# Optimization experiments

Measured on AMD Instinct MI355X. Metric: run time of the kernel, lower is better.

Reference implementation:

```python
import jax, jax.numpy as jnp
import numpy as np


def setup_inputs() -> dict:
    key = jax.random.key(0)
    ks = jax.random.split(key, 8)
    B, T, I, H, O = 4096, 2048, 4, 20, 4
    s_ih = 1.0 / np.sqrt(H)
    return {
        "x": jax.random.normal(ks[0], (B, T, I), dtype=jnp.float32),
        "h0": jax.random.normal(ks[1], (B, H), dtype=jnp.float32),
        "W_ih": jax.random.uniform(ks[2], (H, I), jnp.float32, -s_ih, s_ih),
        "W_hh": jax.random.uniform(ks[3], (H, H), jnp.float32, -s_ih, s_ih),
        "b_ih": jax.random.uniform(ks[4], (H,), jnp.float32, -s_ih, s_ih),
        "b_hh": jax.random.uniform(ks[5], (H,), jnp.float32, -s_ih, s_ih),
        "fc_w": jax.random.uniform(ks[6], (O, H), jnp.float32, -s_ih, s_ih),
        "fc_b": jax.random.uniform(ks[7], (O,), jnp.float32, -s_ih, s_ih),
    }


def reference(x, h0, W_ih, W_hh, b_ih, b_hh, fc_w, fc_b):
    # x: [B, T, I] batch_first; vanilla tanh RNN recurrence.
    # Precompute the input projection for all timesteps in one GEMM.
    xi = jnp.einsum("bti,hi->tbh", x, W_ih) + b_ih + b_hh  # [T, B, H]

    def step(h, xt):
        h = jnp.tanh(xt + h @ W_hh.T)  # [B, H]
        return h, None

    h_last, _ = jax.lax.scan(step, h0, xi)
    # Module takes last timestep only, then Linear(H -> 4).
    return h_last @ fc_w.T + fc_b  # [B, 4]
```

## Files before the change

### kernel.cpp

```cpp
#include <hip/hip_runtime.h>
#include <cstddef>


typedef float f32x2 __attribute__((ext_vector_type(2)));
typedef float f32x4 __attribute__((ext_vector_type(4)));

constexpr int Tn   = 2048;
constexpr int Hn   = 20;
constexpr int EPB  = 16;
constexpr int SB   = 16;
constexpr int NBLK = Tn / SB;

__global__ __launch_bounds__(256, 1) void rnn_fwd(
    const float* __restrict__ x,
    const float* __restrict__ h0,
    const float* __restrict__ W_ih,
    const float* __restrict__ W_hh,
    const float* __restrict__ b_ih,
    const float* __restrict__ b_hh,
    const float* __restrict__ fc_w,
    const float* __restrict__ fc_b,
    float* __restrict__ out)
{
    __shared__ __align__(16) f32x4 xlds[2][EPB][SB + 1];
    __shared__ float hsh[EPB][24];

    const int tid = threadIdx.x;
    const int j   = tid & 15;
    const int e   = tid >> 4;
    const int b   = blockIdx.x * EPB + e;
    const int uB  = 16 + (j & 3);

    const float S = 2.88539008177792681472f;

    f32x2 w2[16];
#pragma unroll
    for (int r = 0; r < 16; ++r) {
        const int k = (j - r) & 15;
        w2[r] = f32x2{S * W_hh[j * Hn + k], S * W_hh[uB * Hn + k]};
    }
    f32x2 wq2[4], xiw[4];
#pragma unroll
    for (int c = 0; c < 4; ++c) {
        wq2[c] = f32x2{S * W_hh[j * Hn + 16 + c], S * W_hh[uB * Hn + 16 + c]};
        xiw[c] = f32x2{S * W_ih[j * 4 + c],       S * W_ih[uB * 4 + c]};
    }
    f32x2 bias2 = f32x2{S * (b_ih[j] + b_hh[j]), S * (b_ih[uB] + b_hh[uB])};

    float hA = h0[b * Hn + j];
    float hB = h0[b * Hn + uB];

    const f32x4* __restrict__ xp =
        reinterpret_cast<const f32x4*>(x) + (size_t)b * Tn;

#define DPPM " row_mask:0xf bank_mask:0xf\n\t"
#define PKB  " op_sel:[0,0,0] op_sel_hi:[1,0,1]\n\t"

#define STEP(XV) do {                                                         \
    f32x2 xa_ = __builtin_shufflevector((XV), (XV), 0, 1);                    \
    f32x2 xb_ = __builtin_shufflevector((XV), (XV), 2, 3);                    \
    asm volatile(                                                             \
                 \
  "v_pk_fma_f32 v[46:47], %[x0], %[xa], %[b2]" PKB                            \
  "v_pk_mul_f32 v[48:49], %[x1], %[xa] op_sel:[0,1] op_sel_hi:[1,1]\n\t"      \
  "v_pk_fma_f32 v[46:47], %[x2], %[xb], v[46:47]" PKB                         \
  "v_pk_fma_f32 v[48:49], %[x3], %[xb], v[48:49] op_sel:[0,1,0] op_sel_hi:[1,1,1]\n\t" \
                                \
  "v_mov_b32 v42, %[hA]\n\t"                                                  \
                   \
  "v_mov_b32_dpp v44, %[hA] row_ror:1"  DPPM                                  \
  "v_pk_fma_f32 v[46:47], %[w0], v[42:43], v[46:47]" PKB                      \
  "v_mov_b32_dpp v42, %[hA] row_ror:2"  DPPM                                  \
  "v_pk_fma_f32 v[48:49], %[w1], v[44:45], v[48:49]" PKB                      \
  "v_mov_b32_dpp v44, %[hA] row_ror:3"  DPPM                                  \
  "v_pk_fma_f32 v[46:47], %[w2], v[42:43], v[46:47]" PKB                      \
  "v_mov_b32_dpp v42, %[hA] row_ror:4"  DPPM                                  \
  "v_pk_fma_f32 v[48:49], %[w3], v[44:45], v[48:49]" PKB                      \
  "v_mov_b32_dpp v44, %[hA] row_ror:5"  DPPM                                  \
  "v_pk_fma_f32 v[46:47], %[w4], v[42:43], v[46:47]" PKB                      \
  "v_mov_b32_dpp v42, %[hA] row_ror:6"  DPPM                                  \
  "v_pk_fma_f32 v[48:49], %[w5], v[44:45], v[48:49]" PKB                      \
  "v_mov_b32_dpp v44, %[hA] row_ror:7"  DPPM                                  \
  "v_pk_fma_f32 v[46:47], %[w6], v[42:43], v[46:47]" PKB                      \
  "v_mov_b32_dpp v42, %[hA] row_ror:8"  DPPM                                  \
  "v_pk_fma_f32 v[48:49], %[w7], v[44:45], v[48:49]" PKB                      \
  "v_mov_b32_dpp v44, %[hA] row_ror:9"  DPPM                                  \
  "v_pk_fma_f32 v[46:47], %[w8], v[42:43], v[46:47]" PKB                      \
  "v_mov_b32_dpp v42, %[hA] row_ror:10" DPPM                                  \
  "v_pk_fma_f32 v[48:49], %[w9], v[44:45], v[48:49]" PKB                      \
  "v_mov_b32_dpp v44, %[hA] row_ror:11" DPPM                                  \
  "v_pk_fma_f32 v[46:47], %[w10], v[42:43], v[46:47]" PKB                     \
  "v_mov_b32_dpp v42, %[hA] row_ror:12" DPPM                                  \
  "v_pk_fma_f32 v[48:49], %[w11], v[44:45], v[48:49]" PKB                     \
  "v_mov_b32_dpp v44, %[hA] row_ror:13" DPPM                                  \
  "v_pk_fma_f32 v[46:47], %[w12], v[42:43], v[46:47]" PKB                     \
  "v_mov_b32_dpp v42, %[hA] row_ror:14" DPPM                                  \
  "v_pk_fma_f32 v[48:49], %[w13], v[44:45], v[48:49]" PKB                     \
  "v_mov_b32_dpp v44, %[hA] row_ror:15" DPPM                                  \
  "v_pk_fma_f32 v[46:47], %[w14], v[42:43], v[46:47]" PKB                     \
  "v_mov_b32_dpp v42, %[hB] quad_perm:[0,0,0,0]" DPPM                         \
  "v_pk_fma_f32 v[48:49], %[w15], v[44:45], v[48:49]" PKB                     \
  "v_mov_b32_dpp v44, %[hB] quad_perm:[1,1,1,1]" DPPM                         \
  "v_pk_fma_f32 v[46:47], %[q0], v[42:43], v[46:47]" PKB                      \
  "v_mov_b32_dpp v42, %[hB] quad_perm:[2,2,2,2]" DPPM                         \
  "v_pk_fma_f32 v[48:49], %[q1], v[44:45], v[48:49]" PKB                      \
  "v_mov_b32_dpp v44, %[hB] quad_perm:[3,3,3,3]" DPPM                         \
  "v_pk_fma_f32 v[46:47], %[q2], v[42:43], v[46:47]" PKB                      \
  "v_pk_fma_f32 v[48:49], %[q3], v[44:45], v[48:49]" PKB                      \
                    \
  "v_pk_add_f32 v[46:47], v[46:47], v[48:49]\n\t"                             \
  "v_exp_f32 v50, v46\n\t"                                                    \
  "v_exp_f32 v51, v47\n\t"                                                    \
  "v_add_f32 v50, 1.0, v50\n\t"                                               \
  "v_add_f32 v51, 1.0, v51\n\t"                                               \
  "v_rcp_f32 v50, v50\n\t"                                                    \
  "v_rcp_f32 v51, v51\n\t"                                                    \
  "v_fma_f32 %[hA], v50, -2.0, 1.0\n\t"                                       \
  "v_fma_f32 %[hB], v51, -2.0, 1.0"                                           \
  : [hA] "+v"(hA), [hB] "+v"(hB)                                              \
  : [xa] "v"(xa_), [xb] "v"(xb_),                                             \
    [w0] "v"(w2[0]),   [w1] "v"(w2[1]),   [w2] "v"(w2[2]),   [w3] "v"(w2[3]), \
    [w4] "v"(w2[4]),   [w5] "v"(w2[5]),   [w6] "v"(w2[6]),   [w7] "v"(w2[7]), \
    [w8] "v"(w2[8]),   [w9] "v"(w2[9]),   [w10] "v"(w2[10]), [w11] "v"(w2[11]),\
    [w12] "v"(w2[12]), [w13] "v"(w2[13]), [w14] "v"(w2[14]), [w15] "v"(w2[15]),\
    [q0] "v"(wq2[0]),  [q1] "v"(wq2[1]),  [q2] "v"(wq2[2]),  [q3] "v"(wq2[3]),\
    [x0] "v"(xiw[0]),  [x1] "v"(xiw[1]),  [x2] "v"(xiw[2]),  [x3] "v"(xiw[3]),\
    [b2] "v"(bias2)                                                           \
  : "v42","v43","v44","v45","v46","v47","v48","v49","v50","v51");             \
} while (0)

    xlds[0][e][j] = xp[j];
    f32x4 q0 = xlds[0][e][0];
    f32x4 q1 = xlds[0][e][1];
    f32x4 q2 = xlds[0][e][2];

    int cur = 0;
#pragma unroll 1
    for (int k = 0; k < NBLK; ++k) {
        const int kn = (k + 1 < NBLK) ? (k + 1) : (NBLK - 1);
        f32x4 xr = xp[kn * SB + j];
        const int nxt = cur ^ 1;
#pragma unroll
        for (int s = 0; s < SB - 3; ++s) {
            f32x4 xv = q0; q0 = q1; q1 = q2;
            q2 = xlds[cur][e][s + 3];
            STEP(xv);
        }
        xlds[nxt][e][j] = xr;
        { f32x4 xv = q0; q0 = q1; q1 = q2; q2 = xlds[nxt][e][0]; STEP(xv); }
        { f32x4 xv = q0; q0 = q1; q1 = q2; q2 = xlds[nxt][e][1]; STEP(xv); }
        { f32x4 xv = q0; q0 = q1; q1 = q2; q2 = xlds[nxt][e][2]; STEP(xv); }
        cur = nxt;
    }
#undef STEP
#undef PKB
#undef DPPM

    hsh[e][j] = hA;
    if (j < 4) hsh[e][16 + j] = hB;
    if (j < 4) {
        float o = fc_b[j];
#pragma unroll
        for (int kk = 0; kk < Hn; ++kk)
            o = __builtin_fmaf(hsh[e][kk], fc_w[j * Hn + kk], o);
        out[b * 4 + j] = o;
    }
}

extern "C" void kernel_launch(void* const* d_in, const int* in_sizes, int n_in,
                              void* d_out, int out_size, void* d_ws, size_t ws_size,
                              hipStream_t stream) {
    const float* x    = (const float*)d_in[0];
    const float* h0   = (const float*)d_in[1];
    const float* W_ih = (const float*)d_in[2];
    const float* W_hh = (const float*)d_in[3];
    const float* b_ih = (const float*)d_in[4];
    const float* b_hh = (const float*)d_in[5];
    const float* fc_w = (const float*)d_in[6];
    const float* fc_b = (const float*)d_in[7];
    float* out = (float*)d_out;

    rnn_fwd<<<dim3(256), dim3(256), 0, stream>>>(x, h0, W_ih, W_hh, b_ih, b_hh,
                                                 fc_w, fc_b, out);
}
```

Baseline: 403.9 us.

## Precompute next step's input projection off the critical path, use four accumulators

Splits each RNN step into a recurrent multiply-accumulate phase and a tail that reduces the partial sums, applies tanh, and immediately seeds the next step's accumulators with that step's input projection and bias. This takes the x·W_ih term off the h-dependent dependency chain. It also spreads the 20 recurrent FMAs across four accumulator pairs instead of two, shortening the serial FMA chain at the cost of extra adds in the reduction. The x prefetch pipeline is shifted by one timestep to match. A risk is that the final x projection computed past the last timestep is wasted work, and the extra accumulator registers add pressure.

```diff
diff --git a/kernel.cpp b/kernel.cpp
--- a/kernel.cpp
+++ b/kernel.cpp
@@ -56,83 +56,98 @@
 #define DPPM " row_mask:0xf bank_mask:0xf\n\t"
 #define PKB  " op_sel:[0,0,0] op_sel_hi:[1,0,1]\n\t"
 
-#define STEP(XV) do {                                                         \
-    f32x2 xa_ = __builtin_shufflevector((XV), (XV), 0, 1);                    \
-    f32x2 xb_ = __builtin_shufflevector((XV), (XV), 2, 3);                    \
+#define STEP_MAC() do {                                                       \
     asm volatile(                                                             \
-                 \
-  "v_pk_fma_f32 v[46:47], %[x0], %[xa], %[b2]" PKB                            \
-  "v_pk_mul_f32 v[48:49], %[x1], %[xa] op_sel:[0,1] op_sel_hi:[1,1]\n\t"      \
-  "v_pk_fma_f32 v[46:47], %[x2], %[xb], v[46:47]" PKB                         \
-  "v_pk_fma_f32 v[48:49], %[x3], %[xb], v[48:49] op_sel:[0,1,0] op_sel_hi:[1,1,1]\n\t" \
-                                \
   "v_mov_b32 v42, %[hA]\n\t"                                                  \
-                   \
   "v_mov_b32_dpp v44, %[hA] row_ror:1"  DPPM                                  \
-  "v_pk_fma_f32 v[46:47], %[w0], v[42:43], v[46:47]" PKB                      \
-  "v_mov_b32_dpp v42, %[hA] row_ror:2"  DPPM                                  \
-  "v_pk_fma_f32 v[48:49], %[w1], v[44:45], v[48:49]" PKB                      \
-  "v_mov_b32_dpp v44, %[hA] row_ror:3"  DPPM                                  \
-  "v_pk_fma_f32 v[46:47], %[w2], v[42:43], v[46:47]" PKB                      \
-  "v_mov_b32_dpp v42, %[hA] row_ror:4"  DPPM                                  \
-  "v_pk_fma_f32 v[48:49], %[w3], v[44:45], v[48:49]" PKB                      \
-  "v_mov_b32_dpp v44, %[hA] row_ror:5"  DPPM                                  \
-  "v_pk_fma_f32 v[46:47], %[w4], v[42:43], v[46:47]" PKB                      \
+  "v_mov_b32_dpp v46, %[hA] row_ror:2"  DPPM                                  \
+  "v_pk_fma_f32 %[P], %[w0], v[42:43], %[P]" PKB                              \
+  "v_mov_b32_dpp v42, %[hA] row_ror:3"  DPPM                                  \
+  "v_pk_fma_f32 %[Q], %[w1], v[44:45], %[Q]" PKB                              \
+  "v_mov_b32_dpp v44, %[hA] row_ror:4"  DPPM                                  \
+  "v_pk_fma_f32 %[R], %[w2], v[46:47], %[R]" PKB                              \
+  "v_mov_b32_dpp v46, %[hA] row_ror:5"  DPPM                                  \
+  "v_pk_fma_f32 %[Sc], %[w3], v[42:43], %[Sc]" PKB                            \
   "v_mov_b32_dpp v42, %[hA] row_ror:6"  DPPM                                  \
-  "v_pk_fma_f32 v[48:49], %[w5], v[44:45], v[48:49]" PKB                      \
+  "v_pk_fma_f32 %[P], %[w4], v[44:45], %[P]" PKB                              \
   "v_mov_b32_dpp v44, %[hA] row_ror:7"  DPPM                                  \
-  "v_pk_fma_f32 v[46:47], %[w6], v[42:43], v[46:47]" PKB                      \
-  "v_mov_b32_dpp v42, %[hA] row_ror:8"  DPPM                                  \
-  "v_pk_fma_f32 v[48:49], %[w7], v[44:45], v[48:49]" PKB                      \
-  "v_mov_b32_dpp v44, %[hA] row_ror:9"  DPPM                                  \
-  "v_pk_fma_f32 v[46:47], %[w8], v[42:43], v[46:47]" PKB                      \
-  "v_mov_b32_dpp v42, %[hA] row_ror:10" DPPM                                  \
-  "v_pk_fma_f32 v[48:49], %[w9], v[44:45], v[48:49]" PKB                      \
-  "v_mov_b32_dpp v44, %[hA] row_ror:11" DPPM                                  \
-  "v_pk_fma_f32 v[46:47], %[w10], v[42:43], v[46:47]" PKB                     \
+  "v_pk_fma_f32 %[Q], %[w5], v[46:47], %[Q]" PKB                              \
+  "v_mov_b32_dpp v46, %[hA] row_ror:8"  DPPM                                  \
+  "v_pk_fma_f32 %[R], %[w6], v[42:43], %[R]" PKB                              \
+  "v_mov_b32_dpp v42, %[hA] row_ror:9"  DPPM                                  \
+  "v_pk_fma_f32 %[Sc], %[w7], v[44:45], %[Sc]" PKB                            \
+  "v_mov_b32_dpp v44, %[hA] row_ror:10" DPPM                                  \
+  "v_pk_fma_f32 %[P], %[w8], v[46:47], %[P]" PKB                              \
+  "v_mov_b32_dpp v46, %[hA] row_ror:11" DPPM                                  \
+  "v_pk_fma_f32 %[Q], %[w9], v[42:43], %[Q]" PKB                              \
   "v_mov_b32_dpp v42, %[hA] row_ror:12" DPPM                                  \
-  "v_pk_fma_f32 v[48:49], %[w11], v[44:45], v[48:49]" PKB                     \
+  "v_pk_fma_f32 %[R], %[w10], v[44:45], %[R]" PKB                             \
   "v_mov_b32_dpp v44, %[hA] row_ror:13" DPPM                                  \
-  "v_pk_fma_f32 v[46:47], %[w12], v[42:43], v[46:47]" PKB                     \
-  "v_mov_b32_dpp v42, %[hA] row_ror:14" DPPM                                  \
-  "v_pk_fma_f32 v[48:49], %[w13], v[44:45], v[48:49]" PKB                     \
-  "v_mov_b32_dpp v44, %[hA] row_ror:15" DPPM                                  \
-  "v_pk_fma_f32 v[46:47], %[w14], v[42:43], v[46:47]" PKB                     \
-  "v_mov_b32_dpp v42, %[hB] quad_perm:[0,0,0,0]" DPPM                         \
-  "v_pk_fma_f32 v[48:49], %[w15], v[44:45], v[48:49]" PKB                     \
-  "v_mov_b32_dpp v44, %[hB] quad_perm:[1,1,1,1]" DPPM                         \
-  "v_pk_fma_f32 v[46:47], %[q0], v[42:43], v[46:47]" PKB                      \
+  "v_pk_fma_f32 %[Sc], %[w11], v[46:47], %[Sc]" PKB                           \
+  "v_mov_b32_dpp v46, %[hA] row_ror:14" DPPM                                  \
+  "v_pk_fma_f32 %[P], %[w12], v[42:43], %[P]" PKB                             \
+  "v_mov_b32_dpp v42, %[hA] row_ror:15" DPPM                                  \
+  "v_pk_fma_f32 %[Q], %[w13], v[44:45], %[Q]" PKB                             \
+  "v_mov_b32_dpp v44, %[hB] quad_perm:[0,0,0,0]" DPPM                         \
+  "v_pk_fma_f32 %[R], %[w14], v[46:47], %[R]" PKB                             \
+  "v_mov_b32_dpp v46, %[hB] quad_perm:[1,1,1,1]" DPPM                         \
+  "v_pk_fma_f32 %[Sc], %[w15], v[42:43], %[Sc]" PKB                           \
   "v_mov_b32_dpp v42, %[hB] quad_perm:[2,2,2,2]" DPPM                         \
-  "v_pk_fma_f32 v[48:49], %[q1], v[44:45], v[48:49]" PKB                      \
+  "v_pk_fma_f32 %[P], %[q0], v[44:45], %[P]" PKB                              \
   "v_mov_b32_dpp v44, %[hB] quad_perm:[3,3,3,3]" DPPM                         \
-  "v_pk_fma_f32 v[46:47], %[q2], v[42:43], v[46:47]" PKB                      \
-  "v_pk_fma_f32 v[48:49], %[q3], v[44:45], v[48:49]" PKB                      \
-                    \
-  "v_pk_add_f32 v[46:47], v[46:47], v[48:49]\n\t"                             \
-  "v_exp_f32 v50, v46\n\t"                                                    \
-  "v_exp_f32 v51, v47\n\t"                                                    \
-  "v_add_f32 v50, 1.0, v50\n\t"                                               \
-  "v_add_f32 v51, 1.0, v51\n\t"                                               \
-  "v_rcp_f32 v50, v50\n\t"                                                    \
-  "v_rcp_f32 v51, v51\n\t"                                                    \
-  "v_fma_f32 %[hA], v50, -2.0, 1.0\n\t"                                       \
-  "v_fma_f32 %[hB], v51, -2.0, 1.0"                                           \
-  : [hA] "+v"(hA), [hB] "+v"(hB)                                              \
-  : [xa] "v"(xa_), [xb] "v"(xb_),                                             \
+  "v_pk_fma_f32 %[Q], %[q1], v[46:47], %[Q]" PKB                              \
+  "v_pk_fma_f32 %[R], %[q2], v[42:43], %[R]" PKB                              \
+  "v_pk_fma_f32 %[Sc], %[q3], v[44:45], %[Sc]"                                \
+  " op_sel:[0,0,0] op_sel_hi:[1,0,1]"                                         \
+  : [P] "+v"(xiP), [Q] "+v"(xiQ), [R] "+v"(xiR), [Sc] "+v"(xiS)               \
+  : [hA] "v"(hA), [hB] "v"(hB),                                               \
     [w0] "v"(w2[0]),   [w1] "v"(w2[1]),   [w2] "v"(w2[2]),   [w3] "v"(w2[3]), \
     [w4] "v"(w2[4]),   [w5] "v"(w2[5]),   [w6] "v"(w2[6]),   [w7] "v"(w2[7]), \
     [w8] "v"(w2[8]),   [w9] "v"(w2[9]),   [w10] "v"(w2[10]), [w11] "v"(w2[11]),\
     [w12] "v"(w2[12]), [w13] "v"(w2[13]), [w14] "v"(w2[14]), [w15] "v"(w2[15]),\
-    [q0] "v"(wq2[0]),  [q1] "v"(wq2[1]),  [q2] "v"(wq2[2]),  [q3] "v"(wq2[3]),\
-    [x0] "v"(xiw[0]),  [x1] "v"(xiw[1]),  [x2] "v"(xiw[2]),  [x3] "v"(xiw[3]),\
+    [q0] "v"(wq2[0]),  [q1] "v"(wq2[1]),  [q2] "v"(wq2[2]),  [q3] "v"(wq2[3]) \
+  : "v42","v43","v44","v45","v46","v47");                                     \
+} while (0)
+
+#define STEP_TAIL(XV) do {                                                    \
+    f32x2 xa_ = __builtin_shufflevector((XV), (XV), 0, 1);                    \
+    f32x2 xb_ = __builtin_shufflevector((XV), (XV), 2, 3);                    \
+    asm volatile(                                                             \
+  "v_pk_add_f32 v[48:49], %[P], %[Q]\n\t"                                     \
+  "v_pk_add_f32 v[50:51], %[R], %[Sc]\n\t"                                    \
+  "v_pk_fma_f32 %[P], %[x0], %[xa], %[b2]" PKB                                \
+  "v_pk_add_f32 v[48:49], v[48:49], v[50:51]\n\t"                             \
+  "v_pk_mul_f32 %[Q], %[x1], %[xa] op_sel:[0,1] op_sel_hi:[1,1]\n\t"          \
+  "v_pk_mul_f32 %[R], %[x2], %[xb] op_sel:[0,0] op_sel_hi:[1,0]\n\t"          \
+  "v_exp_f32 v52, v48\n\t"                                                    \
+  "v_exp_f32 v53, v49\n\t"                                                    \
+  "v_pk_mul_f32 %[Sc], %[x3], %[xb] op_sel:[0,1] op_sel_hi:[1,1]\n\t"         \
+  "v_add_f32 v52, 1.0, v52\n\t"                                               \
+  "v_add_f32 v53, 1.0, v53\n\t"                                               \
+  "v_rcp_f32 v52, v52\n\t"                                                    \
+  "v_rcp_f32 v53, v53\n\t"                                                    \
+  "v_fma_f32 %[hA], v52, -2.0, 1.0\n\t"                                       \
+  "v_fma_f32 %[hB], v53, -2.0, 1.0"                                           \
+  : [hA] "=v"(hA), [hB] "=v"(hB),                                             \
+    [P] "+v"(xiP), [Q] "+v"(xiQ), [R] "+v"(xiR), [Sc] "+v"(xiS)               \
+  : [xa] "v"(xa_), [xb] "v"(xb_),                                             \
+    [x0] "v"(xiw[0]), [x1] "v"(xiw[1]), [x2] "v"(xiw[2]), [x3] "v"(xiw[3]),   \
     [b2] "v"(bias2)                                                           \
-  : "v42","v43","v44","v45","v46","v47","v48","v49","v50","v51");             \
+  : "v48","v49","v50","v51","v52","v53");                                     \
 } while (0)
 
+#define STEP(XV) do { STEP_MAC(); STEP_TAIL(XV); } while (0)
+
     xlds[0][e][j] = xp[j];
-    f32x4 q0 = xlds[0][e][0];
-    f32x4 q1 = xlds[0][e][1];
-    f32x4 q2 = xlds[0][e][2];
+    f32x4 x0v = xp[0];
+    f32x2 xiP = f32x2{__builtin_fmaf(x0v[0], xiw[0][0], bias2[0]),
+                      __builtin_fmaf(x0v[0], xiw[0][1], bias2[1])};
+    f32x2 xiQ = f32x2{x0v[1] * xiw[1][0], x0v[1] * xiw[1][1]};
+    f32x2 xiR = f32x2{x0v[2] * xiw[2][0], x0v[2] * xiw[2][1]};
+    f32x2 xiS = f32x2{x0v[3] * xiw[3][0], x0v[3] * xiw[3][1]};
+    f32x4 q0 = xlds[0][e][1];
+    f32x4 q1 = xlds[0][e][2];
+    f32x4 q2 = xlds[0][e][3];
 
     int cur = 0;
 #pragma unroll 1
@@ -141,18 +156,21 @@
         f32x4 xr = xp[kn * SB + j];
         const int nxt = cur ^ 1;
 #pragma unroll
-        for (int s = 0; s < SB - 3; ++s) {
+        for (int s = 0; s < SB - 4; ++s) {
             f32x4 xv = q0; q0 = q1; q1 = q2;
-            q2 = xlds[cur][e][s + 3];
+            q2 = xlds[cur][e][s + 4];
             STEP(xv);
         }
         xlds[nxt][e][j] = xr;
         { f32x4 xv = q0; q0 = q1; q1 = q2; q2 = xlds[nxt][e][0]; STEP(xv); }
         { f32x4 xv = q0; q0 = q1; q1 = q2; q2 = xlds[nxt][e][1]; STEP(xv); }
         { f32x4 xv = q0; q0 = q1; q1 = q2; q2 = xlds[nxt][e][2]; STEP(xv); }
+        { f32x4 xv = q0; q0 = q1; q1 = q2; q2 = xlds[nxt][e][3]; STEP(xv); }
         cur = nxt;
     }
 #undef STEP
+#undef STEP_MAC
+#undef STEP_TAIL
 #undef PKB
 #undef DPPM
 
```

Result: no change. 400.7 us (-0.8%).
